# Optimization experiments

Measured on AMD Instinct MI355X. Metric: run time of the kernel, lower is better.

Reference implementation:

```python
import jax, jax.numpy as jnp
import numpy as np

N = 13627
E = 504378
D = 500


def _seg_softmax(e, seg, n):
    m = jax.ops.segment_max(e, seg, num_segments=n)
    ex = jnp.exp(e - m[seg])
    s = jax.ops.segment_sum(ex, seg, num_segments=n)
    return ex / (s[seg] + 1e-16)


def _gatv2(x, src, dst, Wl, Wr, att, b, n):
    # PyG GATv2Conv (heads=1): message = Wl x_src; score uses Wl x_src + Wr x_dst
    xl = x @ Wl                                   # [N, F]
    xr = x @ Wr                                   # [N, F]
    e = jax.nn.leaky_relu(xl[src] + xr[dst], 0.2) @ att   # [E]
    a = _seg_softmax(e, dst, n)                   # segment softmax over targets
    out = jax.ops.segment_sum(a[:, None] * xl[src], dst, num_segments=n)
    return out + b


def setup_inputs() -> dict:
    key = jax.random.key(0)
    ks = jax.random.split(key, 24)
    s = 0.05
    inp = {
        'x': jax.random.normal(ks[0], (N, D), dtype=jnp.float32),
        'edge_index': jax.random.randint(ks[1], (2, E), 0, N),
        'neg_edge_index': jax.random.randint(ks[2], (2, E), 0, N),
        'Wl1': jax.random.normal(ks[3], (D, 300)) * s,
        'Wr1': jax.random.normal(ks[4], (D, 300)) * s,
        'att1': jax.random.normal(ks[5], (300,)) * s,
        'b1': jnp.zeros((300,)),
        'Wl2': jax.random.normal(ks[6], (300, 100)) * s,
        'Wr2': jax.random.normal(ks[7], (300, 100)) * s,
        'att2': jax.random.normal(ks[8], (100,)) * s,
        'b2': jnp.zeros((100,)),
        'Wl3': jax.random.normal(ks[9], (100, 1)) * s,
        'Wr3': jax.random.normal(ks[10], (100, 1)) * s,
        'att3': jax.random.normal(ks[11], (1,)) * s,
        'b3': jnp.zeros((1,)),
        'W_lin1': jax.random.normal(ks[12], (D, 100)) * s,
        'b_lin1': jnp.zeros((100,)),
        'W_lin2': jax.random.normal(ks[13], (D, 100)) * s,
        'b_lin2': jnp.zeros((100,)),
        'c1': jnp.array([0.5], dtype=jnp.float32),
        'c2': jnp.array([0.5], dtype=jnp.float32),
    }
    return inp


def reference(x, edge_index, neg_edge_index, Wl1, Wr1, att1, b1, Wl2, Wr2, att2, b2,
              Wl3, Wr3, att3, b3, W_lin1, b_lin1, W_lin2, b_lin2, c1, c2):
    # eval mode: dropout / dropout_adj are identity
    loops = jnp.arange(N)
    src = jnp.concatenate([edge_index[0], loops])   # GATv2Conv adds self loops
    dst = jnp.concatenate([edge_index[1], loops])

    h1 = jax.nn.relu(_gatv2(x, src, dst, Wl1, Wr1, att1, b1, N))
    h2 = jax.nn.relu(_gatv2(h1, src, dst, Wl2, Wr2, att2, b2, N))

    xo = h2 + jax.nn.relu(x @ W_lin1 + b_lin1)
    z = h2 + jax.nn.relu(x @ W_lin2 + b_lin2)

    # link-prediction reconstruction loss
    pos_s = jnp.sum(z[edge_index[0]] * z[edge_index[1]], axis=1)
    pos_loss = -jnp.mean(jnp.log(jax.nn.sigmoid(pos_s) + 1e-15))
    neg_s = jnp.sum(z[neg_edge_index[0]] * z[neg_edge_index[1]], axis=1)
    neg_loss = -jnp.mean(jnp.log(1.0 - jax.nn.sigmoid(neg_s) + 1e-15))
    r_loss = pos_loss + neg_loss

    out = _gatv2(xo, src, dst, Wl3, Wr3, att3, b3, N)   # [N, 1]
    return out, r_loss, c1, c2
```

## Files before the change

### kernel.cpp

```cpp
#include <hip/hip_runtime.h>
#include <hip/hip_bf16.h>

#define NODES 13627
#define DIM   500

typedef short short8 __attribute__((ext_vector_type(8)));
typedef float f32x4 __attribute__((ext_vector_type(4)));
typedef float floatx2 __attribute__((ext_vector_type(2)));

__device__ inline float wave_reduce_sum(float v) {
#pragma unroll
    for (int o = 32; o > 0; o >>= 1) v += __shfl_xor(v, o, 64);
    return v;
}

__device__ inline void store_v(float* p, float v) { *p = v; }
__device__ inline void store_v(__hip_bfloat16* p, float v) { *p = __float2bfloat16(v); }

__device__ inline float blo(unsigned w) { unsigned t = w << 16;        return __builtin_bit_cast(float, t); }
__device__ inline float bhi(unsigned w) { unsigned t = w & 0xffff0000u; return __builtin_bit_cast(float, t); }

__device__ inline unsigned char to_fp8(float v) {
    int r = __builtin_amdgcn_cvt_pk_fp8_f32(v, v, 0, false);
    return (unsigned char)(r & 0xff);
}

__device__ inline unsigned pk2bf(float a, float b) {
    unsigned la = (unsigned)__builtin_bit_cast(unsigned short, __float2bfloat16(a));
    unsigned hb = (unsigned)__builtin_bit_cast(unsigned short, __float2bfloat16(b));
    return la | (hb << 16);
}

struct b4 { __hip_bfloat16 a, b, c, d; };

__global__ __launch_bounds__(256) void hist_kernel(const int* __restrict__ dst,
                                                   int* __restrict__ cnt, int E) {
    int i = blockIdx.x * blockDim.x + threadIdx.x;
    if (i < E) atomicAdd(&cnt[dst[i]], 1);
}

__global__ __launch_bounds__(1024) void scan_kernel(int* __restrict__ cnt_cur,
                                                    int* __restrict__ off, int n) {
    __shared__ int wsum[16];
    const int tid = threadIdx.x, lane = tid & 63, w = tid >> 6;
    int carry = 0;
    for (int base = 0; base < n; base += 1024) {
        int i = base + tid;
        int v = (i < n) ? cnt_cur[i] : 0;
        int s = v;
#pragma unroll
        for (int o = 1; o < 64; o <<= 1) {
            int t = __shfl_up(s, o, 64);
            if (lane >= o) s += t;
        }
        if (lane == 63) wsum[w] = s;
        __syncthreads();
        if (w == 0 && lane < 16) {
            int x = wsum[lane];
            int sx = x;
#pragma unroll
            for (int o = 1; o < 16; o <<= 1) {
                int t = __shfl_up(sx, o, 64);
                if (lane >= o) sx += t;
            }
            wsum[lane] = sx;
        }
        __syncthreads();
        int wo = (w == 0) ? 0 : wsum[w - 1];
        int total = wsum[15];
        int excl = carry + wo + (s - v);
        if (i < n) { off[i] = excl; cnt_cur[i] = excl; }
        carry += total;
        __syncthreads();
    }
    if (tid == 0) off[n] = carry;
}

__global__ __launch_bounds__(256) void scatter_kernel(const int* __restrict__ src,
                                                      const int* __restrict__ dst,
                                                      int* __restrict__ cur,
                                                      int* __restrict__ ssrc, int E) {
    int i = blockIdx.x * blockDim.x + threadIdx.x;
    if (i < E) {
        int p = atomicAdd(&cur[dst[i]], 1);
        ssrc[p] = src[i];
    }
}

__global__ __launch_bounds__(256) void convert_all_kernel(
    const float* __restrict__ x,
    const float* __restrict__ Wl1, const float* __restrict__ Wr1,
    const float* __restrict__ Wl2, const float* __restrict__ Wr2,
    const float* __restrict__ Ws1, const float* __restrict__ Ws2,
    const float* __restrict__ bs1, const float* __restrict__ bs2,
    __hip_bfloat16* __restrict__ W1T, __hip_bfloat16* __restrict__ W2T,
    __hip_bfloat16* __restrict__ WsT, float* __restrict__ bcat,
    __hip_bfloat16* __restrict__ xb, int M) {
    int i = blockIdx.x * 256 + threadIdx.x;
    if (i < 327680) {
        int n = i >> 9, k = i & 511;
        float v = 0.f;
        if (k < 500) {
            if (n < 300) v = Wl1[k * 300 + n];
            else if (n < 600) v = Wr1[k * 300 + n - 300];
        }
        W1T[i] = __float2bfloat16(v);
    } else if (i < 409600) {
        int j = i - 327680;
        int n = j / 320, k = j - n * 320;
        float v = 0.f;
        if (k < 300) {
            if (n < 100) v = Wl2[k * 100 + n];
            else if (n < 200) v = Wr2[k * 100 + n - 100];
        }
        W2T[j] = __float2bfloat16(v);
    } else if (i < 540672) {
        int j = i - 409600;
        int n = j >> 9, k = j & 511;
        float v = 0.f;
        if (k < 500) {
            if (n < 100) v = Ws1[k * 100 + n];
            else if (n < 200) v = Ws2[k * 100 + n - 100];
        }
        WsT[j] = __float2bfloat16(v);
    } else if (i < 540928) {
        int n = i - 540672;
        float v = 0.f;
        if (n < 100) v = bs1[n];
        else if (n < 200) v = bs2[n - 100];
        bcat[n] = v;
    } else {
        int j = i - 540928;
        if (j >= M * 128) return;
        int m = j >> 7, k = (j & 127) << 2;
        b4 o;
        if (k < 500) {
            float4 v = *(const float4*)(x + (size_t)m * 500 + k);
            o.a = __float2bfloat16(v.x); o.b = __float2bfloat16(v.y);
            o.c = __float2bfloat16(v.z); o.d = __float2bfloat16(v.w);
        } else {
            o.a = o.b = o.c = o.d = __float2bfloat16(0.f);
        }
        *(b4*)(xb + (size_t)m * 512 + k) = o;
    }
}

template <int EPI, typename TC>
__global__ __launch_bounds__(256) void mfma_gemm(
    const __hip_bfloat16* __restrict__ A, const __hip_bfloat16* __restrict__ BT,
    TC* __restrict__ C, const float* __restrict__ bias, const float* __restrict__ h2,
    unsigned char* __restrict__ p8, __hip_bfloat16* __restrict__ pb,
    int M, int Kp, int Nn, int ldc) {
    __shared__ short AsF[8 * 64 * 8];
    __shared__ short BsF[4 * 64 * 8];
    const int t = threadIdx.x;
    const int w = t >> 6, lane = t & 63;
    const int c = t & 3, rr = t >> 2;
    const int m0 = blockIdx.y * 128, n0 = blockIdx.x * 64;

    f32x4 acc[2][4];
#pragma unroll
    for (int i = 0; i < 2; i++)
#pragma unroll
        for (int j = 0; j < 4; j++) acc[i][j] = (f32x4){0.f, 0.f, 0.f, 0.f};

    for (int k0 = 0; k0 < Kp; k0 += 32) {
#pragma unroll
        for (int r = 0; r < 2; r++) {
            int m = r * 64 + rr;
            int gm = m0 + m; if (gm >= M) gm = M - 1;
            float4 v = *(const float4*)(A + (size_t)gm * Kp + k0 + c * 8);
            int mi = m >> 4, sl = m & 15;
            *(float4*)(&AsF[(mi * 64 + c * 16 + sl) * 8]) = v;
        }
        {
            int n = rr;
            float4 v = *(const float4*)(BT + (size_t)(n0 + n) * Kp + k0 + c * 8);
            int ni = n >> 4, sl = n & 15;
            *(float4*)(&BsF[(ni * 64 + c * 16 + sl) * 8]) = v;
        }
        __syncthreads();
        short8 a0 = *(const short8*)(&AsF[((w * 2 + 0) * 64 + lane) * 8]);
        short8 a1 = *(const short8*)(&AsF[((w * 2 + 1) * 64 + lane) * 8]);
#pragma unroll
        for (int j = 0; j < 4; j++) {
            short8 b = *(const short8*)(&BsF[(j * 64 + lane) * 8]);
            acc[0][j] = __builtin_amdgcn_mfma_f32_16x16x32_bf16(a0, b, acc[0][j], 0, 0, 0);
            acc[1][j] = __builtin_amdgcn_mfma_f32_16x16x32_bf16(a1, b, acc[1][j], 0, 0, 0);
        }
        __syncthreads();
    }

    const int q = lane >> 4, sl = lane & 15;
#pragma unroll
    for (int i = 0; i < 2; i++) {
#pragma unroll
        for (int j = 0; j < 4; j++) {
#pragma unroll
            for (int reg = 0; reg < 4; reg++) {
                int gm = m0 + w * 32 + i * 16 + q * 4 + reg;
                int gn = n0 + j * 16 + sl;
                if (gm >= M) continue;
                float v = acc[i][j][reg];
                if constexpr (EPI == 1) {
                    if (gn < 300)       p8[(size_t)gm * 304 + gn] = to_fp8(v);
                    else if (gn < 600)  pb[(size_t)gm * 320 + (gn - 300)] = __float2bfloat16(v);
                    else if (gn < 620)  pb[(size_t)gm * 320 + (gn - 300)] = __float2bfloat16(0.f);
                    else if (gn < 624)  p8[(size_t)gm * 304 + (gn - 320)] = 0;
                } else if constexpr (EPI == 2) {
                    if (gn < 100)       p8[(size_t)gm * 112 + gn] = to_fp8(v);
                    else if (gn < 200)  pb[(size_t)gm * 128 + (gn - 100)] = __float2bfloat16(v);
                    else if (gn < 212)  p8[(size_t)gm * 112 + (gn - 100)] = 0;
                    else if (gn < 240)  pb[(size_t)gm * 128 + (gn - 112)] = __float2bfloat16(0.f);
                } else if constexpr (EPI == 3) {
                    if (gn < 200) {
                        int cn = gn < 100 ? gn : gn - 100;
                        float val = fmaxf(v + bias[gn], 0.f) + h2[(size_t)gm * 100 + cn];
                        if (gn < 100) C[(size_t)gm * 100 + gn] = val;
                        else p8[(size_t)gm * 128 + (gn - 100)] = to_fp8(val);
                    } else if (gn < 228) {
                        p8[(size_t)gm * 128 + (gn - 100)] = 0;
                    }
                } else {
                    store_v(&C[(size_t)gm * ldc + gn], v);
                }
            }
        }
    }
}

template <int F, int NJ, int SL8, int SRB, int SOUT, int JSL, typename TOUT>
__global__ __launch_bounds__(256) void gat_f8_kernel(
    const unsigned char* __restrict__ xl8, const __hip_bfloat16* __restrict__ xrb,
    const float* __restrict__ att, const float* __restrict__ bias,
    const int* __restrict__ off, const int* __restrict__ ssrc,
    TOUT* __restrict__ out, int n) {
    const int t = threadIdx.x;
    const int lane = t & 63;
    const int sl = lane & 15, q = lane >> 4;
    int wid = blockIdx.x * 4 + (t >> 6);
    if (wid >= n) wid = n - 1;

    floatx2 attv[NJ * 2], xrv[NJ * 2], acc[NJ * 2];
    const unsigned* xru = (const unsigned*)xrb + (size_t)wid * (SRB / 2);
#pragma unroll
    for (int j = 0; j < NJ; j++) {
        const int f0 = sl * 4 + j * 64;
        if (f0 < F) {
            float4 a4 = *(const float4*)(att + f0);
            attv[j * 2 + 0] = (floatx2){a4.x, a4.y};
            attv[j * 2 + 1] = (floatx2){a4.z, a4.w};
        } else {
            attv[j * 2 + 0] = (floatx2){0.f, 0.f};
            attv[j * 2 + 1] = (floatx2){0.f, 0.f};
        }
        unsigned u0 = __builtin_nontemporal_load(xru + (f0 >> 1));
        unsigned u1 = __builtin_nontemporal_load(xru + (f0 >> 1) + 1);
        xrv[j * 2 + 0] = (floatx2){blo(u0), bhi(u0)};
        xrv[j * 2 + 1] = (floatx2){blo(u1), bhi(u1)};
        acc[j * 2 + 0] = (floatx2){0.f, 0.f};
        acc[j * 2 + 1] = (floatx2){0.f, 0.f};
    }

    const int s0 = off[wid], s1 = off[wid + 1];
    const int eb = s0 - 1;
    const int ee = s1;
    float den = 0.f;
    const int myoff = sl * 4;

    int srcB;
    unsigned u[NJ];
    {
        int eq0 = eb + q;
        int srcA = wid;
        if (eq0 >= s0 && eq0 < ee) srcA = __builtin_nontemporal_load(ssrc + eq0);
        int eq1 = eb + 4 + q;
        srcB = wid;
        if (eq1 >= s0 && eq1 < ee) srcB = __builtin_nontemporal_load(ssrc + eq1);
        const unsigned char* row = xl8 + (size_t)srcA * SL8;
#pragma unroll
        for (int j = 0; j < NJ; j++) {
            const bool ld = (j < NJ - 1) || (sl < JSL);
            u[j] = ld ? *(const unsigned*)(row + myoff + j * 64) : 0u;
        }
    }

    for (int e0 = eb; e0 < ee; e0 += 4) {
        const bool act = (e0 + q) < ee;
        int srcC = wid;
        {
            int eq2 = e0 + 8 + q;
            if (eq2 >= s0 && eq2 < ee) srcC = __builtin_nontemporal_load(ssrc + eq2);
        }
        unsigned un[NJ];
        {
            const unsigned char* row1 = xl8 + (size_t)srcB * SL8;
#pragma unroll
            for (int j = 0; j < NJ; j++) {
                const bool ld = (j < NJ - 1) || (sl < JSL);
                un[j] = ld ? *(const unsigned*)(row1 + myoff + j * 64) : 0u;
            }
        }
        floatx2 xlv[NJ * 2];
        floatx2 p2 = (floatx2){0.f, 0.f};
#pragma unroll
        for (int j = 0; j < NJ; j++) {
            floatx2 lo = __builtin_amdgcn_cvt_pk_f32_fp8((int)u[j], false);
            floatx2 hi = __builtin_amdgcn_cvt_pk_f32_fp8((int)u[j], true);
            xlv[j * 2 + 0] = lo;
            xlv[j * 2 + 1] = hi;
            floatx2 s0v = lo + xrv[j * 2 + 0];
            floatx2 s1v = hi + xrv[j * 2 + 1];
            floatx2 g0 = __builtin_elementwise_max(s0v, 0.2f * s0v);
            floatx2 g1 = __builtin_elementwise_max(s1v, 0.2f * s1v);
            p2 += attv[j * 2 + 0] * g0;
            p2 += attv[j * 2 + 1] * g1;
        }
        float p = p2.x + p2.y;
        p += __shfl_xor(p, 1, 64);
        p += __shfl_xor(p, 2, 64);
        p += __shfl_xor(p, 4, 64);
        p += __shfl_xor(p, 8, 64);
        float ex = act ? expf(p) : 0.f;
        den += ex;
        floatx2 ex2 = (floatx2){ex, ex};
#pragma unroll
        for (int i = 0; i < NJ * 2; i++) acc[i] += ex2 * xlv[i];
#pragma unroll
        for (int j = 0; j < NJ; j++) u[j] = un[j];
        srcB = srcC;
    }

    float* af = (float*)acc;
#pragma unroll
    for (int o = 16; o <= 32; o <<= 1) {
        den += __shfl_xor(den, o, 64);
#pragma unroll
        for (int i = 0; i < NJ * 4; i++) af[i] += __shfl_xor(af[i], o, 64);
    }

    if (q == 0) {
        const float inv = 1.f / (den + 1e-16f);
#pragma unroll
        for (int j = 0; j < NJ; j++) {
            const int f0 = sl * 4 + j * 64;
            if (f0 >= SOUT) continue;
            float r[4];
#pragma unroll
            for (int cc = 0; cc < 4; cc++) {
                const int f = f0 + cc;
                float v = 0.f;
                if (f < F) v = fmaxf(af[j * 4 + cc] * inv + bias[f], 0.f);
                r[cc] = v;
            }
            if constexpr (sizeof(TOUT) == 4) {
                *(float4*)((float*)out + (size_t)wid * SOUT + f0) =
                    make_float4(r[0], r[1], r[2], r[3]);
            } else {
                unsigned* op = (unsigned*)out + (size_t)wid * (SOUT / 2) + (f0 >> 1);
                op[0] = pk2bf(r[0], r[1]);
                op[1] = pk2bf(r[2], r[3]);
            }
        }
    }
}

__global__ __launch_bounds__(256) void gemm_vec1_kernel(
    const float* __restrict__ xo, const float* __restrict__ wl,
    const float* __restrict__ wr, float* __restrict__ xl3,
    float* __restrict__ xr3, int M, int ldx) {
    const int wid = blockIdx.x * 4 + (threadIdx.x >> 6);
    const int lane = threadIdx.x & 63;
    if (wid >= M) return;
    float a = 0.f, b = 0.f;
    for (int f = lane; f < 100; f += 64) {
        float v = xo[(size_t)wid * ldx + f];
        a += v * wl[f];
        b += v * wr[f];
    }
    a = wave_reduce_sum(a);
    b = wave_reduce_sum(b);
    if (lane == 0) { xl3[wid] = a; xr3[wid] = b; }
}

__global__ __launch_bounds__(256) void gat3_kernel(
    const float* __restrict__ xl3, const float* __restrict__ xr3,
    const float* __restrict__ att3, const float* __restrict__ b3,
    const int* __restrict__ off, const int* __restrict__ ssrc,
    float* __restrict__ out, int n) {
    const int wid = blockIdx.x * 4 + (threadIdx.x >> 6);
    const int lane = threadIdx.x & 63;
    if (wid >= n) return;
    const float xrv = xr3[wid];
    const float att = att3[0];
    float num = 0.f, den = 0.f;
    const int s0 = off[wid], s1 = off[wid + 1];
    for (int e = s0 - 1 + lane; e < s1; e += 64) {
        int src = (e < s0) ? wid : ssrc[e];
        float xlv = xl3[src];
        float t = xlv + xrv;
        float g = t > 0.f ? t : 0.2f * t;
        float ex = expf(g * att);
        den += ex;
        num += ex * xlv;
    }
    num = wave_reduce_sum(num);
    den = wave_reduce_sum(den);
    if (lane == 0) out[wid] = num / (den + 1e-16f) + b3[0];
}

__global__ __launch_bounds__(256) void loss_kernel(
    const unsigned char* __restrict__ z8, const int* __restrict__ pos,
    const int* __restrict__ neg, float* __restrict__ part, int nb, int E) {
    const int lane = threadIdx.x & 63;
    const int sl = lane & 15;
    const int wlocal = threadIdx.x >> 6;
    const int q = lane >> 4;
    const int nq = gridDim.x * 16;
    const int qid = (blockIdx.x * 4 + wlocal) * 4 + q;
    const int total = 2 * E;
    float psum = 0.f, nsum = 0.f;

    for (int base = qid; base < total; base += 4 * nq) {
        uint2 au[4], bu[4];
        bool act[4], isN[4];
#pragma unroll
        for (int s = 0; s < 4; s++) {
            int it = base + s * nq;
            act[s] = it < total;
            int itc = act[s] ? it : 0;
            isN[s] = itc >= E;
            int e = isN[s] ? itc - E : itc;
            const int* ei = isN[s] ? neg : pos;
            int u = ei[e], v = ei[E + e];
            au[s] = *(const uint2*)(z8 + (size_t)u * 128 + sl * 8);
            bu[s] = *(const uint2*)(z8 + (size_t)v * 128 + sl * 8);
        }
#pragma unroll
        for (int s = 0; s < 4; s++) {
            floatx2 a0 = __builtin_amdgcn_cvt_pk_f32_fp8((int)au[s].x, false);
            floatx2 a1 = __builtin_amdgcn_cvt_pk_f32_fp8((int)au[s].x, true);
            floatx2 a2 = __builtin_amdgcn_cvt_pk_f32_fp8((int)au[s].y, false);
            floatx2 a3 = __builtin_amdgcn_cvt_pk_f32_fp8((int)au[s].y, true);
            floatx2 b0 = __builtin_amdgcn_cvt_pk_f32_fp8((int)bu[s].x, false);
            floatx2 b1 = __builtin_amdgcn_cvt_pk_f32_fp8((int)bu[s].x, true);
            floatx2 b2 = __builtin_amdgcn_cvt_pk_f32_fp8((int)bu[s].y, false);
            floatx2 b3 = __builtin_amdgcn_cvt_pk_f32_fp8((int)bu[s].y, true);
            float p = a0.x * b0.x + a0.y * b0.y + a1.x * b1.x + a1.y * b1.y
                    + a2.x * b2.x + a2.y * b2.y + a3.x * b3.x + a3.y * b3.y;
            p += __shfl_xor(p, 1, 64);
            p += __shfl_xor(p, 2, 64);
            p += __shfl_xor(p, 4, 64);
            p += __shfl_xor(p, 8, 64);
            if (sl == 0 && act[s]) {
                float sig = 1.f / (1.f + expf(-p));
                if (isN[s]) nsum += logf(1.f - sig + 1e-15f);
                else        psum += logf(sig + 1e-15f);
            }
        }
    }
    float pw = wave_reduce_sum(psum);
    float nw = wave_reduce_sum(nsum);
    __shared__ float sp[4], sn[4];
    if (lane == 0) { sp[wlocal] = pw; sn[wlocal] = nw; }
    __syncthreads();
    if (threadIdx.x == 0) {
        part[blockIdx.x]      = sp[0] + sp[1] + sp[2] + sp[3];
        part[nb + blockIdx.x] = sn[0] + sn[1] + sn[2] + sn[3];
    }
}

__global__ __launch_bounds__(1024) void finalize_kernel(
    const float* __restrict__ part, int nb,
    const float* __restrict__ c1, const float* __restrict__ c2,
    float* __restrict__ out, int n, int E) {
    __shared__ float sp[16], sn[16];
    const int tid = threadIdx.x, lane = tid & 63, w = tid >> 6;
    float p = 0.f, q = 0.f;
    for (int i = tid; i < nb; i += 1024) { p += part[i]; q += part[nb + i]; }
    p = wave_reduce_sum(p);
    q = wave_reduce_sum(q);
    if (lane == 0) { sp[w] = p; sn[w] = q; }
    __syncthreads();
    if (tid == 0) {
        float tp = 0.f, tq = 0.f;
#pragma unroll
        for (int i = 0; i < 16; i++) { tp += sp[i]; tq += sn[i]; }
        out[n]     = -(tp + tq) / (float)E;
        out[n + 1] = c1[0];
        out[n + 2] = c2[0];
    }
}

extern "C" void kernel_launch(void* const* d_in, const int* in_sizes, int n_in,
                              void* d_out, int out_size, void* d_ws, size_t ws_size,
                              hipStream_t stream) {
    const float* x      = (const float*)d_in[0];
    const int*   ei     = (const int*)d_in[1];
    const int*   nei    = (const int*)d_in[2];
    const float* Wl1    = (const float*)d_in[3];
    const float* Wr1    = (const float*)d_in[4];
    const float* att1   = (const float*)d_in[5];
    const float* b1     = (const float*)d_in[6];
    const float* Wl2    = (const float*)d_in[7];
    const float* Wr2    = (const float*)d_in[8];
    const float* att2   = (const float*)d_in[9];
    const float* b2     = (const float*)d_in[10];
    const float* Wl3    = (const float*)d_in[11];
    const float* Wr3    = (const float*)d_in[12];
    const float* att3   = (const float*)d_in[13];
    const float* b3     = (const float*)d_in[14];
    const float* Wlin1  = (const float*)d_in[15];
    const float* blin1  = (const float*)d_in[16];
    const float* Wlin2  = (const float*)d_in[17];
    const float* blin2  = (const float*)d_in[18];
    const float* c1     = (const float*)d_in[19];
    const float* c2     = (const float*)d_in[20];
    float* out = (float*)d_out;

    const int E = in_sizes[1] / 2;
    const int N = NODES;
    const int LOSS_BLOCKS = 4096;

    char* ws = (char*)d_ws;
    unsigned char*  xl8  = (unsigned char*)(ws + 0);
    unsigned char*  xl28 = (unsigned char*)(ws + 0);
    __hip_bfloat16* xrb  = (__hip_bfloat16*)(ws + 4194304);
    __hip_bfloat16* xr2b = (__hip_bfloat16*)(ws + 4194304);
    float*          xo   = (float*)(ws + 4194304);
    unsigned char*  z8   = (unsigned char*)(ws + 9645312);
    __hip_bfloat16* h1b  = (__hip_bfloat16*)(ws + 12915712);
    float*          h2   = (float*)(ws + 12915712);
    __hip_bfloat16* xb   = (__hip_bfloat16*)(ws + 21637120);
    __hip_bfloat16* W1T  = (__hip_bfloat16*)(ws + 35591168);
    __hip_bfloat16* W2T  = (__hip_bfloat16*)(ws + 36246528);
    __hip_bfloat16* WsT  = (__hip_bfloat16*)(ws + 36410368);
    float*          bcat = (float*)(ws + 36672512);
    float*          xl3  = (float*)(ws + 36673536);
    float*          xr3  = (float*)(ws + 36728064);
    int*            ioff = (int*)(ws + 36782592);
    int*            cur  = (int*)(ws + 36837376);
    int*            ssrc = (int*)(ws + 36892160);
    float*          part = (float*)(ws + 38909952);

    hipMemsetAsync(cur, 0, sizeof(int) * N, stream);

    hist_kernel<<<(E + 255) / 256, 256, 0, stream>>>(ei + E, cur, E);
    scan_kernel<<<1, 1024, 0, stream>>>(cur, ioff, N);
    scatter_kernel<<<(E + 255) / 256, 256, 0, stream>>>(ei, ei + E, cur, ssrc, E);

    convert_all_kernel<<<(540928 + N * 128 + 255) / 256, 256, 0, stream>>>(
        x, Wl1, Wr1, Wl2, Wr2, Wlin1, Wlin2, blin1, blin2,
        W1T, W2T, WsT, bcat, xb, N);

    mfma_gemm<1, __hip_bfloat16><<<dim3(10, 107), 256, 0, stream>>>(
        xb, W1T, (__hip_bfloat16*)nullptr, nullptr, nullptr, xl8, xrb, N, 512, 640, 0);
    gat_f8_kernel<300, 5, 304, 320, 320, 11, __hip_bfloat16>
        <<<(N + 3) / 4, 256, 0, stream>>>(xl8, xrb, att1, b1, ioff, ssrc, h1b, N);

    mfma_gemm<2, __hip_bfloat16><<<dim3(4, 107), 256, 0, stream>>>(
        h1b, W2T, (__hip_bfloat16*)nullptr, nullptr, nullptr, xl28, xr2b, N, 320, 256, 0);
    gat_f8_kernel<100, 2, 112, 128, 100, 9, float>
        <<<(N + 3) / 4, 256, 0, stream>>>(xl28, xr2b, att2, b2, ioff, ssrc, h2, N);

    mfma_gemm<3, float><<<dim3(4, 107), 256, 0, stream>>>(
        xb, WsT, xo, bcat, h2, z8, nullptr, N, 512, 256, 0);

    loss_kernel<<<LOSS_BLOCKS, 256, 0, stream>>>(z8, ei, nei, part, LOSS_BLOCKS, E);

    gemm_vec1_kernel<<<(N + 3) / 4, 256, 0, stream>>>(xo, Wl3, Wr3, xl3, xr3, N, 100);
    gat3_kernel<<<(N + 3) / 4, 256, 0, stream>>>(xl3, xr3, att3, b3, ioff, ssrc, out, N);

    finalize_kernel<<<1, 1024, 0, stream>>>(part, LOSS_BLOCKS, c1, c2, out, N, E);
}
```

Before: 376.7 us.

## Process two destination nodes per wave in GAT aggregation with interleaved gathers

The GAT fp8 aggregation kernel now uses 64-thread blocks where each wave handles two destination nodes at once. The gather loads and prefetches for both nodes are interleaved, which doubles the memory-level parallelism per wave and is meant to hide gather latency. The cost is about twice the register use (launch_bounds 64,3), and the shorter-degree node wastes idle iterations until the longer one finishes. Separately, expf and logf in gat3 and the loss kernel are replaced with fast intrinsics (__expf, __logf, rcp), trading a little accuracy for cheaper transcendentals.

```diff
diff --git a/kernel.cpp b/kernel.cpp
--- a/kernel.cpp
+++ b/kernel.cpp
@@ -230,19 +230,20 @@
 }
 
 template <int F, int NJ, int SL8, int SRB, int SOUT, int JSL, typename TOUT>
-__global__ __launch_bounds__(256) void gat_f8_kernel(
+__global__ __launch_bounds__(64, 3) void gat_f8_kernel(
     const unsigned char* __restrict__ xl8, const __hip_bfloat16* __restrict__ xrb,
     const float* __restrict__ att, const float* __restrict__ bias,
     const int* __restrict__ off, const int* __restrict__ ssrc,
     TOUT* __restrict__ out, int n) {
-    const int t = threadIdx.x;
-    const int lane = t & 63;
+    const int lane = threadIdx.x;
     const int sl = lane & 15, q = lane >> 4;
-    int wid = blockIdx.x * 4 + (t >> 6);
-    if (wid >= n) wid = n - 1;
-
-    floatx2 attv[NJ * 2], xrv[NJ * 2], acc[NJ * 2];
-    const unsigned* xru = (const unsigned*)xrb + (size_t)wid * (SRB / 2);
+    const int widA = blockIdx.x * 2;
+    int widB = widA + 1;
+    if (widB >= n) widB = n - 1;
+
+    floatx2 attv[NJ * 2], xrvA[NJ * 2], xrvB[NJ * 2], accA[NJ * 2], accB[NJ * 2];
+    const unsigned* xruA = (const unsigned*)xrb + (size_t)widA * (SRB / 2);
+    const unsigned* xruB = (const unsigned*)xrb + (size_t)widB * (SRB / 2);
 #pragma unroll
     for (int j = 0; j < NJ; j++) {
         const int f0 = sl * 4 + j * 64;
@@ -254,112 +255,170 @@
             attv[j * 2 + 0] = (floatx2){0.f, 0.f};
             attv[j * 2 + 1] = (floatx2){0.f, 0.f};
         }
-        unsigned u0 = __builtin_nontemporal_load(xru + (f0 >> 1));
-        unsigned u1 = __builtin_nontemporal_load(xru + (f0 >> 1) + 1);
-        xrv[j * 2 + 0] = (floatx2){blo(u0), bhi(u0)};
-        xrv[j * 2 + 1] = (floatx2){blo(u1), bhi(u1)};
-        acc[j * 2 + 0] = (floatx2){0.f, 0.f};
-        acc[j * 2 + 1] = (floatx2){0.f, 0.f};
-    }
-
-    const int s0 = off[wid], s1 = off[wid + 1];
-    const int eb = s0 - 1;
-    const int ee = s1;
-    float den = 0.f;
+        unsigned a0 = __builtin_nontemporal_load(xruA + (f0 >> 1));
+        unsigned a1 = __builtin_nontemporal_load(xruA + (f0 >> 1) + 1);
+        xrvA[j * 2 + 0] = (floatx2){blo(a0), bhi(a0)};
+        xrvA[j * 2 + 1] = (floatx2){blo(a1), bhi(a1)};
+        unsigned b0 = __builtin_nontemporal_load(xruB + (f0 >> 1));
+        unsigned b1 = __builtin_nontemporal_load(xruB + (f0 >> 1) + 1);
+        xrvB[j * 2 + 0] = (floatx2){blo(b0), bhi(b0)};
+        xrvB[j * 2 + 1] = (floatx2){blo(b1), bhi(b1)};
+        accA[j * 2 + 0] = (floatx2){0.f, 0.f};
+        accA[j * 2 + 1] = (floatx2){0.f, 0.f};
+        accB[j * 2 + 0] = (floatx2){0.f, 0.f};
+        accB[j * 2 + 1] = (floatx2){0.f, 0.f};
+    }
+
+    const int sA0 = off[widA], eeA = off[widA + 1];
+    const int sB0 = off[widB], eeB = off[widB + 1];
+    const int ebA = sA0 - 1, ebB = sB0 - 1;
+    float denA = 0.f, denB = 0.f;
     const int myoff = sl * 4;
 
-    int srcB;
-    unsigned u[NJ];
+    const int itCntA = (eeA - ebA + 3) >> 2;
+    const int itCntB = (eeB - ebB + 3) >> 2;
+    const int itMax = itCntA > itCntB ? itCntA : itCntB;
+
+    int srcA1, srcB1;
+    unsigned uA[NJ], uB[NJ];
     {
-        int eq0 = eb + q;
-        int srcA = wid;
-        if (eq0 >= s0 && eq0 < ee) srcA = __builtin_nontemporal_load(ssrc + eq0);
-        int eq1 = eb + 4 + q;
-        srcB = wid;
-        if (eq1 >= s0 && eq1 < ee) srcB = __builtin_nontemporal_load(ssrc + eq1);
-        const unsigned char* row = xl8 + (size_t)srcA * SL8;
+        int eq = ebA + q;
+        int sA = widA; if (eq >= sA0 && eq < eeA) sA = __builtin_nontemporal_load(ssrc + eq);
+        eq = ebA + 4 + q;
+        srcA1 = widA; if (eq >= sA0 && eq < eeA) srcA1 = __builtin_nontemporal_load(ssrc + eq);
+        eq = ebB + q;
+        int sB = widB; if (eq >= sB0 && eq < eeB) sB = __builtin_nontemporal_load(ssrc + eq);
+        eq = ebB + 4 + q;
+        srcB1 = widB; if (eq >= sB0 && eq < eeB) srcB1 = __builtin_nontemporal_load(ssrc + eq);
+        const unsigned char* rA = xl8 + (size_t)sA * SL8;
+        const unsigned char* rB = xl8 + (size_t)sB * SL8;
 #pragma unroll
         for (int j = 0; j < NJ; j++) {
             const bool ld = (j < NJ - 1) || (sl < JSL);
-            u[j] = ld ? *(const unsigned*)(row + myoff + j * 64) : 0u;
-        }
-    }
-
-    for (int e0 = eb; e0 < ee; e0 += 4) {
-        const bool act = (e0 + q) < ee;
-        int srcC = wid;
+            uA[j] = ld ? *(const unsigned*)(rA + myoff + j * 64) : 0u;
+            uB[j] = ld ? *(const unsigned*)(rB + myoff + j * 64) : 0u;
+        }
+    }
+
+    for (int it = 0; it < itMax; ++it) {
+        const int e0A = ebA + it * 4, e0B = ebB + it * 4;
+        int srcA2 = widA;
+        { int eq = e0A + 8 + q; if (eq >= sA0 && eq < eeA) srcA2 = __builtin_nontemporal_load(ssrc + eq); }
+        int srcB2 = widB;
+        { int eq = e0B + 8 + q; if (eq >= sB0 && eq < eeB) srcB2 = __builtin_nontemporal_load(ssrc + eq); }
+        unsigned unA[NJ], unB[NJ];
         {
-            int eq2 = e0 + 8 + q;
-            if (eq2 >= s0 && eq2 < ee) srcC = __builtin_nontemporal_load(ssrc + eq2);
-        }
-        unsigned un[NJ];
-        {
-            const unsigned char* row1 = xl8 + (size_t)srcB * SL8;
+            const unsigned char* rA = xl8 + (size_t)srcA1 * SL8;
+            const unsigned char* rB = xl8 + (size_t)srcB1 * SL8;
 #pragma unroll
             for (int j = 0; j < NJ; j++) {
                 const bool ld = (j < NJ - 1) || (sl < JSL);
-                un[j] = ld ? *(const unsigned*)(row1 + myoff + j * 64) : 0u;
-            }
-        }
-        floatx2 xlv[NJ * 2];
-        floatx2 p2 = (floatx2){0.f, 0.f};
-#pragma unroll
-        for (int j = 0; j < NJ; j++) {
-            floatx2 lo = __builtin_amdgcn_cvt_pk_f32_fp8((int)u[j], false);
-            floatx2 hi = __builtin_amdgcn_cvt_pk_f32_fp8((int)u[j], true);
-            xlv[j * 2 + 0] = lo;
-            xlv[j * 2 + 1] = hi;
-            floatx2 s0v = lo + xrv[j * 2 + 0];
-            floatx2 s1v = hi + xrv[j * 2 + 1];
-            floatx2 g0 = __builtin_elementwise_max(s0v, 0.2f * s0v);
-            floatx2 g1 = __builtin_elementwise_max(s1v, 0.2f * s1v);
-            p2 += attv[j * 2 + 0] * g0;
-            p2 += attv[j * 2 + 1] * g1;
-        }
-        float p = p2.x + p2.y;
-        p += __shfl_xor(p, 1, 64);
-        p += __shfl_xor(p, 2, 64);
-        p += __shfl_xor(p, 4, 64);
-        p += __shfl_xor(p, 8, 64);
-        float ex = act ? expf(p) : 0.f;
-        den += ex;
-        floatx2 ex2 = (floatx2){ex, ex};
-#pragma unroll
-        for (int i = 0; i < NJ * 2; i++) acc[i] += ex2 * xlv[i];
-#pragma unroll
-        for (int j = 0; j < NJ; j++) u[j] = un[j];
-        srcB = srcC;
-    }
-
-    float* af = (float*)acc;
+                unA[j] = ld ? *(const unsigned*)(rA + myoff + j * 64) : 0u;
+                unB[j] = ld ? *(const unsigned*)(rB + myoff + j * 64) : 0u;
+            }
+        }
+        {
+            floatx2 p2 = (floatx2){0.f, 0.f};
+#pragma unroll
+            for (int j = 0; j < NJ; j++) {
+                floatx2 lo = __builtin_amdgcn_cvt_pk_f32_fp8((int)uA[j], false);
+                floatx2 hi = __builtin_amdgcn_cvt_pk_f32_fp8((int)uA[j], true);
+                floatx2 s0v = lo + xrvA[j * 2 + 0];
+                floatx2 s1v = hi + xrvA[j * 2 + 1];
+                floatx2 g0 = __builtin_elementwise_max(s0v, 0.2f * s0v);
+                floatx2 g1 = __builtin_elementwise_max(s1v, 0.2f * s1v);
+                p2 += attv[j * 2 + 0] * g0;
+                p2 += attv[j * 2 + 1] * g1;
+            }
+            float p = p2.x + p2.y;
+            p += __shfl_xor(p, 1, 64);
+            p += __shfl_xor(p, 2, 64);
+            p += __shfl_xor(p, 4, 64);
+            p += __shfl_xor(p, 8, 64);
+            float ex = ((e0A + q) < eeA) ? __expf(p) : 0.f;
+            denA += ex;
+            floatx2 ex2 = (floatx2){ex, ex};
+#pragma unroll
+            for (int j = 0; j < NJ; j++) {
+                floatx2 lo = __builtin_amdgcn_cvt_pk_f32_fp8((int)uA[j], false);
+                floatx2 hi = __builtin_amdgcn_cvt_pk_f32_fp8((int)uA[j], true);
+                accA[j * 2 + 0] += ex2 * lo;
+                accA[j * 2 + 1] += ex2 * hi;
+            }
+        }
+        {
+            floatx2 p2 = (floatx2){0.f, 0.f};
+#pragma unroll
+            for (int j = 0; j < NJ; j++) {
+                floatx2 lo = __builtin_amdgcn_cvt_pk_f32_fp8((int)uB[j], false);
+                floatx2 hi = __builtin_amdgcn_cvt_pk_f32_fp8((int)uB[j], true);
+                floatx2 s0v = lo + xrvB[j * 2 + 0];
+                floatx2 s1v = hi + xrvB[j * 2 + 1];
+                floatx2 g0 = __builtin_elementwise_max(s0v, 0.2f * s0v);
+                floatx2 g1 = __builtin_elementwise_max(s1v, 0.2f * s1v);
+                p2 += attv[j * 2 + 0] * g0;
+                p2 += attv[j * 2 + 1] * g1;
+            }
+            float p = p2.x + p2.y;
+            p += __shfl_xor(p, 1, 64);
+            p += __shfl_xor(p, 2, 64);
+            p += __shfl_xor(p, 4, 64);
+            p += __shfl_xor(p, 8, 64);
+            float ex = ((e0B + q) < eeB) ? __expf(p) : 0.f;
+            denB += ex;
+            floatx2 ex2 = (floatx2){ex, ex};
+#pragma unroll
+            for (int j = 0; j < NJ; j++) {
+                floatx2 lo = __builtin_amdgcn_cvt_pk_f32_fp8((int)uB[j], false);
+                floatx2 hi = __builtin_amdgcn_cvt_pk_f32_fp8((int)uB[j], true);
+                accB[j * 2 + 0] += ex2 * lo;
+                accB[j * 2 + 1] += ex2 * hi;
+            }
+        }
+#pragma unroll
+        for (int j = 0; j < NJ; j++) { uA[j] = unA[j]; uB[j] = unB[j]; }
+        srcA1 = srcA2; srcB1 = srcB2;
+    }
+
+    float* afA = (float*)accA;
+    float* afB = (float*)accB;
 #pragma unroll
     for (int o = 16; o <= 32; o <<= 1) {
-        den += __shfl_xor(den, o, 64);
-#pragma unroll
-        for (int i = 0; i < NJ * 4; i++) af[i] += __shfl_xor(af[i], o, 64);
+        denA += __shfl_xor(denA, o, 64);
+        denB += __shfl_xor(denB, o, 64);
+#pragma unroll
+        for (int i = 0; i < NJ * 4; i++) {
+            afA[i] += __shfl_xor(afA[i], o, 64);
+            afB[i] += __shfl_xor(afB[i], o, 64);
+        }
     }
 
     if (q == 0) {
-        const float inv = 1.f / (den + 1e-16f);
+        const float invA = 1.f / (denA + 1e-16f);
+        const float invB = 1.f / (denB + 1e-16f);
 #pragma unroll
         for (int j = 0; j < NJ; j++) {
             const int f0 = sl * 4 + j * 64;
             if (f0 >= SOUT) continue;
-            float r[4];
+            float rA[4], rB[4];
 #pragma unroll
             for (int cc = 0; cc < 4; cc++) {
                 const int f = f0 + cc;
-                float v = 0.f;
-                if (f < F) v = fmaxf(af[j * 4 + cc] * inv + bias[f], 0.f);
-                r[cc] = v;
+                rA[cc] = (f < F) ? fmaxf(afA[j * 4 + cc] * invA + bias[f], 0.f) : 0.f;
+                rB[cc] = (f < F) ? fmaxf(afB[j * 4 + cc] * invB + bias[f], 0.f) : 0.f;
             }
             if constexpr (sizeof(TOUT) == 4) {
-                *(float4*)((float*)out + (size_t)wid * SOUT + f0) =
-                    make_float4(r[0], r[1], r[2], r[3]);
+                *(float4*)((float*)out + (size_t)widA * SOUT + f0) =
+                    make_float4(rA[0], rA[1], rA[2], rA[3]);
+                *(float4*)((float*)out + (size_t)widB * SOUT + f0) =
+                    make_float4(rB[0], rB[1], rB[2], rB[3]);
             } else {
-                unsigned* op = (unsigned*)out + (size_t)wid * (SOUT / 2) + (f0 >> 1);
-                op[0] = pk2bf(r[0], r[1]);
-                op[1] = pk2bf(r[2], r[3]);
+                unsigned* opA = (unsigned*)out + (size_t)widA * (SOUT / 2) + (f0 >> 1);
+                opA[0] = pk2bf(rA[0], rA[1]);
+                opA[1] = pk2bf(rA[2], rA[3]);
+                unsigned* opB = (unsigned*)out + (size_t)widB * (SOUT / 2) + (f0 >> 1);
+                opB[0] = pk2bf(rB[0], rB[1]);
+                opB[1] = pk2bf(rB[2], rB[3]);
             }
         }
     }
@@ -400,7 +459,7 @@
         float xlv = xl3[src];
         float t = xlv + xrv;
         float g = t > 0.f ? t : 0.2f * t;
-        float ex = expf(g * att);
+        float ex = __expf(g * att);
         den += ex;
         num += ex * xlv;
     }
@@ -453,9 +512,9 @@
             p += __shfl_xor(p, 4, 64);
             p += __shfl_xor(p, 8, 64);
             if (sl == 0 && act[s]) {
-                float sig = 1.f / (1.f + expf(-p));
-                if (isN[s]) nsum += logf(1.f - sig + 1e-15f);
-                else        psum += logf(sig + 1e-15f);
+                float sig = __builtin_amdgcn_rcpf(1.f + __expf(-p));
+                if (isN[s]) nsum += __logf(1.f - sig + 1e-15f);
+                else        psum += __logf(sig + 1e-15f);
             }
         }
     }
@@ -556,12 +615,12 @@
     mfma_gemm<1, __hip_bfloat16><<<dim3(10, 107), 256, 0, stream>>>(
         xb, W1T, (__hip_bfloat16*)nullptr, nullptr, nullptr, xl8, xrb, N, 512, 640, 0);
     gat_f8_kernel<300, 5, 304, 320, 320, 11, __hip_bfloat16>
-        <<<(N + 3) / 4, 256, 0, stream>>>(xl8, xrb, att1, b1, ioff, ssrc, h1b, N);
+        <<<(N + 1) / 2, 64, 0, stream>>>(xl8, xrb, att1, b1, ioff, ssrc, h1b, N);
 
     mfma_gemm<2, __hip_bfloat16><<<dim3(4, 107), 256, 0, stream>>>(
         h1b, W2T, (__hip_bfloat16*)nullptr, nullptr, nullptr, xl28, xr2b, N, 320, 256, 0);
     gat_f8_kernel<100, 2, 112, 128, 100, 9, float>
-        <<<(N + 3) / 4, 256, 0, stream>>>(xl28, xr2b, att2, b2, ioff, ssrc, h2, N);
+        <<<(N + 1) / 2, 64, 0, stream>>>(xl28, xr2b, att2, b2, ioff, ssrc, h2, N);
 
     mfma_gemm<3, float><<<dim3(4, 107), 256, 0, stream>>>(
         xb, WsT, xo, bcat, h2, z8, nullptr, N, 512, 256, 0);
```

Result: slower. 392.9 us (+4.3%).
